# Kernel optimization log

Measured on AMD Instinct MI355X. Metric: run time of the kernel, lower is better.

## Reference

```python
import jax, jax.numpy as jnp
import numpy as np

EPS = 1e-5

def _layernorm(x, g, b):
    mu = jnp.mean(x, axis=-1, keepdims=True)
    var = jnp.mean(jnp.square(x - mu), axis=-1, keepdims=True)
    return (x - mu) * jax.lax.rsqrt(var + EPS) * g + b

def setup_inputs() -> dict:
    key = jax.random.key(0)
    B, N, C, MID = 1, 512, 128, 128
    ks = jax.random.split(key, 12)
    s_c = 1.0 / np.sqrt(C)
    s_m = 1.0 / np.sqrt(MID)
    return {
        "act": jax.random.normal(ks[0], (B, N, N, C), dtype=jnp.float32),
        "mask": jnp.ones((B, N, N), dtype=jnp.float32),
        # input LayerNorm
        "ln_in_g": jnp.ones((C,), jnp.float32),
        "ln_in_b": jnp.zeros((C,), jnp.float32),
        # left/right projections and gates (Linear: y = x @ W + b)
        "wl": jax.random.normal(ks[1], (C, MID), jnp.float32) * s_c,
        "bl": jnp.zeros((MID,), jnp.float32),
        "wr": jax.random.normal(ks[2], (C, MID), jnp.float32) * s_c,
        "br": jnp.zeros((MID,), jnp.float32),
        "wgl": jax.random.normal(ks[3], (C, MID), jnp.float32) * s_c,
        "bgl": jnp.zeros((MID,), jnp.float32),
        "wgr": jax.random.normal(ks[4], (C, MID), jnp.float32) * s_c,
        "bgr": jnp.zeros((MID,), jnp.float32),
        # output gating linear (C -> C)
        "wgate": jax.random.normal(ks[5], (C, C), jnp.float32) * s_c,
        "bgate": jnp.zeros((C,), jnp.float32),
        # center LayerNorm (over MID)
        "ln_c_g": jnp.ones((MID,), jnp.float32),
        "ln_c_b": jnp.zeros((MID,), jnp.float32),
        # output projection (MID -> C)
        "wout": jax.random.normal(ks[6], (MID, C), jnp.float32) * s_m,
        "bout": jnp.zeros((C,), jnp.float32),
    }

def reference(act, mask, ln_in_g, ln_in_b, wl, bl, wr, br, wgl, bgl, wgr, bgr,
              wgate, bgate, ln_c_g, ln_c_b, wout, bout):
    x = _layernorm(act, ln_in_g, ln_in_b)          # [B,N,N,C]
    m = mask[..., None]                             # [B,N,N,1]
    left_proj = m * (x @ wl + bl) * jax.nn.sigmoid(x @ wgl + bgl)   # [B,N,N,MID]
    right_proj = m * (x @ wr + br) * jax.nn.sigmoid(x @ wgr + bgr)  # [B,N,N,MID]
    gate_values = x @ wgate + bgate                 # [B,N,N,C]
    # triangle outgoing: contract over k (second index of both)
    out = jnp.einsum('bikc,bjkc->bijc', left_proj, right_proj)      # [B,N,N,MID]
    out = _layernorm(out, ln_c_g, ln_c_b)
    out = out @ wout + bout                         # [B,N,N,C]
    return out * jax.nn.sigmoid(gate_values)
```

## Files before the change

kernel.cpp:

```cpp
#include <hip/hip_runtime.h>

#define NPOS 512
#define NN_ (512 * 512)

typedef unsigned short u16;
typedef __attribute__((ext_vector_type(8))) short bf16x8_t;
typedef __attribute__((ext_vector_type(4))) float f32x4_t;

__device__ __forceinline__ float bf2f(u16 u) {
  union { unsigned int i; float f; } v;
  v.i = ((unsigned int)u) << 16;
  return v.f;
}
__device__ __forceinline__ u16 f2bf(float f) {
  __bf16 h = (__bf16)f;
  return __builtin_bit_cast(unsigned short, h);
}
__device__ __forceinline__ float sigm(float x) { return 1.0f / (1.0f + __expf(-x)); }

__device__ __forceinline__ void gld_lds16(u16* lds, const u16* g) {
  __builtin_amdgcn_global_load_lds(
      (const __attribute__((address_space(1))) unsigned int*)g,
      (__attribute__((address_space(3))) unsigned int*)lds, 16, 0, 0);
}

__global__ __launch_bounds__(256) void k0_wt(const float* __restrict__ wl,
                                             const float* __restrict__ wgl,
                                             const float* __restrict__ wr,
                                             const float* __restrict__ wgr,
                                             const float* __restrict__ wgate,
                                             u16* __restrict__ wtbase) {
  int b = blockIdx.x;
  int wi = b >> 3;
  int o0 = (b & 7) * 16;
  const float* W = wi == 0 ? wl : wi == 1 ? wgl : wi == 2 ? wr : wi == 3 ? wgr : wgate;
  u16* dst = wtbase + wi * 16384;
  int t = threadIdx.x;
  int o = o0 + (t >> 4);
  int k0 = (t & 15) * 8;
  float v[8];
#pragma unroll
  for (int i = 0; i < 8; ++i) v[i] = W[(k0 + i) * 128 + o];
  ushort4 a, b4;
  a.x = f2bf(v[0]); a.y = f2bf(v[1]); a.z = f2bf(v[2]); a.w = f2bf(v[3]);
  b4.x = f2bf(v[4]); b4.y = f2bf(v[5]); b4.z = f2bf(v[6]); b4.w = f2bf(v[7]);
  *(ushort4*)(dst + o * 128 + k0) = a;
  *(ushort4*)(dst + o * 128 + k0 + 4) = b4;
}

__global__ __launch_bounds__(256) void k0b(const float* __restrict__ wout,
                                           u16* __restrict__ Wt6) {
  int o = blockIdx.x * 16 + (threadIdx.x >> 4);
  int k0 = (threadIdx.x & 15) * 8;
  float v[8];
#pragma unroll
  for (int i = 0; i < 8; ++i) v[i] = wout[(k0 + i) * 128 + o];
  ushort4 a, b4;
  a.x = f2bf(v[0]); a.y = f2bf(v[1]); a.z = f2bf(v[2]); a.w = f2bf(v[3]);
  b4.x = f2bf(v[4]); b4.y = f2bf(v[5]); b4.z = f2bf(v[6]); b4.w = f2bf(v[7]);
  *(ushort4*)(Wt6 + o * 128 + k0) = a;
  *(ushort4*)(Wt6 + o * 128 + k0 + 4) = b4;
}

__global__ __launch_bounds__(512, 4) void k2_fused(
    const float* __restrict__ act, const float* __restrict__ mask,
    const u16* __restrict__ wtbase,
    const float* __restrict__ ln_g, const float* __restrict__ ln_b,
    const float* __restrict__ bl, const float* __restrict__ bgl,
    const float* __restrict__ br, const float* __restrict__ bgr,
    const float* __restrict__ bgate,
    u16* __restrict__ Lt, u16* __restrict__ Rt, u16* __restrict__ Gs) {
  __shared__ __align__(16) unsigned char smem[65536];
  u16* xn  = (u16*)smem;
  u16* wh0 = (u16*)(smem + 32768);
  u16* wh1 = (u16*)(smem + 49152);

  int tid = threadIdx.x;
  int l = tid & 63, w = tid >> 6;
  int wr_ = w >> 1, wc = w & 1;
  int lr = l & 15, lk = l >> 4;
  size_t p0 = (size_t)blockIdx.x * 128;

#define STAGE(i_, buf_)                                                     \
  {                                                                         \
    const u16* src = wtbase + ((i_) >> 1) * 16384 + ((i_) & 1) * 8192;      \
    _Pragma("unroll") for (int q = 0; q < 2; ++q) {                         \
      int s = q * 512 + tid;                                                \
      int row = s >> 4, j = (s & 15) ^ (row & 7);                           \
      gld_lds16((buf_) + s * 8, src + row * 128 + j * 8);                   \
    }                                                                       \
  }
#define ZERO(ACC)                                                           \
  { ACC[0][0] = (f32x4_t){0.f, 0.f, 0.f, 0.f};                              \
    ACC[0][1] = (f32x4_t){0.f, 0.f, 0.f, 0.f};                              \
    ACC[1][0] = (f32x4_t){0.f, 0.f, 0.f, 0.f};                              \
    ACC[1][1] = (f32x4_t){0.f, 0.f, 0.f, 0.f}; }
#define MFK(buf_, ACC, KT, AF0, AF1)                                        \
  {                                                                         \
    int kb = (KT) * 4 + lk;                                                 \
    int o0_ = wc * 32 + lr, o1_ = wc * 32 + 16 + lr;                        \
    bf16x8_t bfr0 = *(const bf16x8_t*)((buf_) + o0_ * 128 + ((kb ^ (o0_ & 7)) * 8)); \
    bf16x8_t bfr1 = *(const bf16x8_t*)((buf_) + o1_ * 128 + ((kb ^ (o1_ & 7)) * 8)); \
    ACC[0][0] = __builtin_amdgcn_mfma_f32_16x16x32_bf16(AF0, bfr0, ACC[0][0], 0, 0, 0); \
    ACC[0][1] = __builtin_amdgcn_mfma_f32_16x16x32_bf16(AF0, bfr1, ACC[0][1], 0, 0, 0); \
    ACC[1][0] = __builtin_amdgcn_mfma_f32_16x16x32_bf16(AF1, bfr0, ACC[1][0], 0, 0, 0); \
    ACC[1][1] = __builtin_amdgcn_mfma_f32_16x16x32_bf16(AF1, bfr1, ACC[1][1], 0, 0, 0); \
  }
#define MF(buf_, ACC)                                                       \
  MFK(buf_, ACC, 0, af00, af10)                                             \
  MFK(buf_, ACC, 1, af01, af11)                                             \
  MFK(buf_, ACC, 2, af02, af12)                                             \
  MFK(buf_, ACC, 3, af03, af13)
#define EPW(ACCP, ACCG, Bp_, Bg_, obase_, ob_)                              \
  {                                                                         \
    float bpv[2], bgv[2];                                                   \
    _Pragma("unroll") for (int n = 0; n < 2; ++n) {                         \
      int og = (obase_) + wc * 32 + n * 16 + lr;                            \
      bpv[n] = Bp_[og]; bgv[n] = Bg_[og];                                   \
    }                                                                       \
    _Pragma("unroll") for (int m = 0; m < 2; ++m) {                         \
      int p4 = wr_ * 32 + m * 16 + lk * 4;                                  \
      float4 mk = *(const float4*)(mask + p0 + p4);                         \
      int slot = p4 >> 3, off = p4 & 7;                                     \
      _Pragma("unroll") for (int n = 0; n < 2; ++n) {                       \
        int ol = wc * 32 + n * 16 + lr;                                     \
        ushort4 v;                                                          \
        v.x = f2bf(mk.x * (ACCP[m][n][0] + bpv[n]) * sigm(ACCG[m][n][0] + bgv[n])); \
        v.y = f2bf(mk.y * (ACCP[m][n][1] + bpv[n]) * sigm(ACCG[m][n][1] + bgv[n])); \
        v.z = f2bf(mk.z * (ACCP[m][n][2] + bpv[n]) * sigm(ACCG[m][n][2] + bgv[n])); \
        v.w = f2bf(mk.w * (ACCP[m][n][3] + bpv[n]) * sigm(ACCG[m][n][3] + bgv[n])); \
        *(ushort4*)((ob_) + ol * 128 + ((slot ^ (ol & 7)) << 3) + off) = v; \
      }                                                                     \
    }                                                                       \
  }
#define EPS(Tdst_, obase_, ob_)                                             \
  {                                                                         \
    _Pragma("unroll") for (int it = 0; it < 2; ++it) {                      \
      int s = it * 512 + tid;                                               \
      int ol = s >> 4, c8 = s & 15;                                         \
      *(uint4*)(Tdst_ + (size_t)((obase_) + ol) * NN_ + p0 + c8 * 8) =      \
          *(const uint4*)((ob_) + ol * 128 + ((c8 ^ (ol & 7)) << 3));       \
    }                                                                       \
  }

  STAGE(0, wh0);
  STAGE(1, wh1);

#pragma unroll
  for (int r = 0; r < 8; ++r) {
    int f = r * 512 + tid;
    int pos = f >> 5, c4 = f & 31;
    float4 v = *(const float4*)(act + (p0 + pos) * 128 + c4 * 4);
    float s1 = v.x + v.y + v.z + v.w;
    float s2 = v.x * v.x + v.y * v.y + v.z * v.z + v.w * v.w;
#pragma unroll
    for (int m = 1; m < 32; m <<= 1) {
      s1 += __shfl_xor(s1, m);
      s2 += __shfl_xor(s2, m);
    }
    float mu = s1 * (1.0f / 128.0f);
    float rstd = rsqrtf(s2 * (1.0f / 128.0f) - mu * mu + 1e-5f);
    int cb = c4 * 4;
    float4 gg = *(const float4*)(ln_g + cb);
    float4 bb = *(const float4*)(ln_b + cb);
    ushort4 o4;
    o4.x = f2bf((v.x - mu) * rstd * gg.x + bb.x);
    o4.y = f2bf((v.y - mu) * rstd * gg.y + bb.y);
    o4.z = f2bf((v.z - mu) * rstd * gg.z + bb.z);
    o4.w = f2bf((v.w - mu) * rstd * gg.w + bb.w);
    int c8 = c4 >> 1, off = (c4 & 1) * 4;
    *(ushort4*)(xn + pos * 128 + ((c8 ^ (pos & 7)) << 3) + off) = o4;
  }
  __syncthreads();

  bf16x8_t af00, af01, af02, af03, af10, af11, af12, af13;
  {
    int row0 = wr_ * 32 + lr;
    int row1 = wr_ * 32 + 16 + lr;
    const u16* x0 = xn + row0 * 128;
    const u16* x1 = xn + row1 * 128;
    af00 = *(const bf16x8_t*)(x0 + (((0 * 4 + lk) ^ (row0 & 7)) * 8));
    af01 = *(const bf16x8_t*)(x0 + (((1 * 4 + lk) ^ (row0 & 7)) * 8));
    af02 = *(const bf16x8_t*)(x0 + (((2 * 4 + lk) ^ (row0 & 7)) * 8));
    af03 = *(const bf16x8_t*)(x0 + (((3 * 4 + lk) ^ (row0 & 7)) * 8));
    af10 = *(const bf16x8_t*)(x1 + (((0 * 4 + lk) ^ (row1 & 7)) * 8));
    af11 = *(const bf16x8_t*)(x1 + (((1 * 4 + lk) ^ (row1 & 7)) * 8));
    af12 = *(const bf16x8_t*)(x1 + (((2 * 4 + lk) ^ (row1 & 7)) * 8));
    af13 = *(const bf16x8_t*)(x1 + (((3 * 4 + lk) ^ (row1 & 7)) * 8));
  }

  f32x4_t apA[2][2], apB[2][2], agA[2][2], agB[2][2];

  ZERO(apA); MF(wh0, apA);
  __syncthreads();
  STAGE(2, wh0);
  ZERO(apB); MF(wh1, apB);
  __syncthreads();
  STAGE(3, wh1);
  ZERO(agA); MF(wh0, agA);
  __syncthreads();
  STAGE(4, wh0);
  ZERO(agB); MF(wh1, agB);
  __syncthreads();
  EPW(apA, agA, bl, bgl, 0, wh1);
  __syncthreads();
  EPS(Lt, 0, wh1);
  __syncthreads();
  EPW(apB, agB, bl, bgl, 64, wh1);
  __syncthreads();
  EPS(Lt, 64, wh1);
  __syncthreads();

  STAGE(5, wh1);
  ZERO(apA); MF(wh0, apA);
  __syncthreads();
  STAGE(6, wh0);
  ZERO(apB); MF(wh1, apB);
  __syncthreads();
  STAGE(7, wh1);
  ZERO(agA); MF(wh0, agA);
  __syncthreads();
  STAGE(8, wh0);
  ZERO(agB); MF(wh1, agB);
  __syncthreads();
  EPW(apA, agA, br, bgr, 0, wh1);
  __syncthreads();
  EPS(Rt, 0, wh1);
  __syncthreads();
  EPW(apB, agB, br, bgr, 64, wh1);
  __syncthreads();
  EPS(Rt, 64, wh1);
  __syncthreads();

  STAGE(9, wh1);
  ZERO(apA); MF(wh0, apA);
  __syncthreads();
  ZERO(apB); MF(wh1, apB);
  __syncthreads();
  {
    u16* ob128 = wh0;
#pragma unroll
    for (int m = 0; m < 2; ++m) {
      int p4 = wr_ * 32 + m * 16 + lk * 4;
      int slot = p4 >> 3, off = p4 & 7;
#pragma unroll
      for (int n = 0; n < 2; ++n) {
        int oA = wc * 32 + n * 16 + lr;
        int oB = 64 + oA;
        float bA = bgate[oA], bB = bgate[oB];
        ushort4 vA, vB;
        vA.x = f2bf(apA[m][n][0] + bA); vA.y = f2bf(apA[m][n][1] + bA);
        vA.z = f2bf(apA[m][n][2] + bA); vA.w = f2bf(apA[m][n][3] + bA);
        vB.x = f2bf(apB[m][n][0] + bB); vB.y = f2bf(apB[m][n][1] + bB);
        vB.z = f2bf(apB[m][n][2] + bB); vB.w = f2bf(apB[m][n][3] + bB);
        *(ushort4*)(ob128 + oA * 128 + ((slot ^ (oA & 7)) << 3) + off) = vA;
        *(ushort4*)(ob128 + oB * 128 + ((slot ^ (oB & 7)) << 3) + off) = vB;
      }
    }
    __syncthreads();
#pragma unroll
    for (int it = 0; it < 4; ++it) {
      int s = it * 512 + tid;
      int o = s >> 4, c8 = s & 15;
      *(uint4*)(Gs + (size_t)o * NN_ + p0 + c8 * 8) =
          *(const uint4*)(ob128 + o * 128 + ((c8 ^ (o & 7)) << 3));
    }
  }
#undef STAGE
#undef ZERO
#undef MFK
#undef MF
#undef EPW
#undef EPS
}

__global__ __launch_bounds__(256, 4) void k3_einsum_mfma(const u16* __restrict__ Lt,
                                                         const u16* __restrict__ Rt,
                                                         u16* __restrict__ Ot) {
  __shared__ __align__(16) u16 smem[2 * 128 * 64];
  u16* La = smem;
  u16* Rb = smem + 128 * 64;

  int tid = threadIdx.x;
  int bid = blockIdx.x;
  int swz = (bid & 7) * 256 + (bid >> 3);
  int c = swz >> 4;
  int t = swz & 15;
  int i0 = (t >> 2) << 7, j0 = (t & 3) << 7;
  const u16* Lg = Lt + (size_t)c * NN_ + (size_t)i0 * 512;
  const u16* Rg = Rt + (size_t)c * NN_ + (size_t)j0 * 512;

  int l = tid & 63, w = tid >> 6;
  int wr = w >> 1, wc = w & 1;
  int lr = l & 15, lk = l >> 4;

  f32x4_t acc[4][4];
#pragma unroll
  for (int m = 0; m < 4; ++m)
#pragma unroll
    for (int n = 0; n < 4; ++n) acc[m][n] = (f32x4_t){0.f, 0.f, 0.f, 0.f};

  for (int kt = 0; kt < 512; kt += 64) {
#pragma unroll
    for (int q = 0; q < 4; ++q) {
      int s = q * 256 + tid;
      int row = s >> 3;
      int k8 = (s & 7) ^ (row & 7);
      gld_lds16(La + s * 8, Lg + (size_t)row * 512 + kt + k8 * 8);
      gld_lds16(Rb + s * 8, Rg + (size_t)row * 512 + kt + k8 * 8);
    }
    __syncthreads();

#pragma unroll
    for (int ks = 0; ks < 2; ++ks) {
      int kb = ks * 4 + lk;
      bf16x8_t af[4], bf[4];
#pragma unroll
      for (int m = 0; m < 4; ++m) {
        int row = wr * 64 + m * 16 + lr;
        af[m] = *(const bf16x8_t*)(La + row * 64 + ((kb ^ (row & 7)) * 8));
      }
#pragma unroll
      for (int n = 0; n < 4; ++n) {
        int row = wc * 64 + n * 16 + lr;
        bf[n] = *(const bf16x8_t*)(Rb + row * 64 + ((kb ^ (row & 7)) * 8));
      }
#pragma unroll
      for (int m = 0; m < 4; ++m)
#pragma unroll
        for (int n = 0; n < 4; ++n)
          acc[m][n] = __builtin_amdgcn_mfma_f32_16x16x32_bf16(af[m], bf[n], acc[m][n], 0, 0, 0);
    }
    __syncthreads();
  }

  u16* ob = smem;
#pragma unroll
  for (int m = 0; m < 4; ++m) {
    int row0 = wr * 64 + m * 16 + lk * 4;
#pragma unroll
    for (int n = 0; n < 4; ++n) {
      int col = (wc * 64 + n * 16 + lr) ^ (lk << 4);
#pragma unroll
      for (int r = 0; r < 4; ++r)
        ob[(row0 + r) * 128 + col] = f2bf(acc[m][n][r]);
    }
  }
  __syncthreads();
#pragma unroll
  for (int it = 0; it < 8; ++it) {
    int s = it * 256 + tid;
    int row = s >> 4, c8 = s & 15;
    int g = (row >> 2) & 3;
    const u16* src = ob + row * 128 + ((c8 * 8) ^ (g << 4));
    *(uint4*)(Ot + (size_t)c * NN_ + (size_t)(i0 + row) * 512 + j0 + c8 * 8) =
        *(const uint4*)src;
  }
}

__global__ __launch_bounds__(512, 4) void k4_mfma(const u16* __restrict__ Ot,
                                                  const u16* __restrict__ Gs,
                                                  const u16* __restrict__ Wt6,
                                                  const float* __restrict__ gc,
                                                  const float* __restrict__ bc,
                                                  const float* __restrict__ bout,
                                                  float* __restrict__ out) {
  __shared__ __align__(16) unsigned char smem[70656];
  u16* ot = (u16*)smem;
  u16* ws = (u16*)(smem + 32768);
  float* ps = (float*)(smem + 65536);
  float* pss = (float*)(smem + 67584);
  float2* munr = (float2*)(smem + 69632);

  int tid = threadIdx.x;
  int l = tid & 63, w = tid >> 6;
  int wr = w >> 1, wc = w & 1;
  int lr = l & 15, lk = l >> 4;
  size_t p0 = (size_t)blockIdx.x * 128;
  int i_row = (int)(p0 >> 9);
  int j0 = (int)(p0 & 511);

#pragma unroll
  for (int q = 0; q < 4; ++q) {
    int s = q * 512 + tid;
    int cc = s >> 4, j = s & 15;
    gld_lds16(ot + s * 8, Ot + (size_t)cc * NN_ + (size_t)i_row * 512 + j0 + j * 8);
  }
#pragma unroll
  for (int q = 0; q < 4; ++q) {
    int s = q * 512 + tid;
    int o = s >> 4, j = (s & 15) ^ (o & 7);
    gld_lds16(ws + s * 8, Wt6 + o * 128 + j * 8);
  }
  __syncthreads();

  int g = tid >> 7, pos = tid & 127;
  float vals[32];
  float s1 = 0.0f, s2 = 0.0f;
#pragma unroll
  for (int m = 0; m < 32; ++m) {
    float v = bf2f(ot[(g * 32 + m) * 128 + pos]);
    vals[m] = v;
    s1 += v;
    s2 += v * v;
  }
  ps[g * 128 + pos] = s1;
  pss[g * 128 + pos] = s2;
  __syncthreads();
  if (tid < 128) {
    float a = ps[tid] + ps[128 + tid] + ps[256 + tid] + ps[384 + tid];
    float b = pss[tid] + pss[128 + tid] + pss[256 + tid] + pss[384 + tid];
    float mu = a * (1.0f / 128.0f);
    float rstd = rsqrtf(b * (1.0f / 128.0f) - mu * mu + 1e-5f);
    munr[tid] = make_float2(mu, rstd);
  }
  __syncthreads();
  float2 mr = munr[pos];

  u16* xn = ot;
#pragma unroll
  for (int mm = 0; mm < 4; ++mm) {
    int c8 = g * 4 + mm;
    ushort4 va, vb;
    int cb = c8 * 8;
    va.x = f2bf((vals[mm * 8 + 0] - mr.x) * mr.y * gc[cb + 0] + bc[cb + 0]);
    va.y = f2bf((vals[mm * 8 + 1] - mr.x) * mr.y * gc[cb + 1] + bc[cb + 1]);
    va.z = f2bf((vals[mm * 8 + 2] - mr.x) * mr.y * gc[cb + 2] + bc[cb + 2]);
    va.w = f2bf((vals[mm * 8 + 3] - mr.x) * mr.y * gc[cb + 3] + bc[cb + 3]);
    vb.x = f2bf((vals[mm * 8 + 4] - mr.x) * mr.y * gc[cb + 4] + bc[cb + 4]);
    vb.y = f2bf((vals[mm * 8 + 5] - mr.x) * mr.y * gc[cb + 5] + bc[cb + 5]);
    vb.z = f2bf((vals[mm * 8 + 6] - mr.x) * mr.y * gc[cb + 6] + bc[cb + 6]);
    vb.w = f2bf((vals[mm * 8 + 7] - mr.x) * mr.y * gc[cb + 7] + bc[cb + 7]);
    int slot = (c8 ^ (pos & 7)) * 8;
    *(ushort4*)(xn + pos * 128 + slot) = va;
    *(ushort4*)(xn + pos * 128 + slot + 4) = vb;
  }
  __syncthreads();

  f32x4_t acc[2][4];
#pragma unroll
  for (int m = 0; m < 2; ++m)
#pragma unroll
    for (int n = 0; n < 4; ++n) acc[m][n] = (f32x4_t){0.f, 0.f, 0.f, 0.f};

#pragma unroll
  for (int kt = 0; kt < 4; ++kt) {
    int kb = kt * 4 + lk;
    bf16x8_t af[2], bf[4];
#pragma unroll
    for (int m = 0; m < 2; ++m) {
      int row = wr * 32 + m * 16 + lr;
      af[m] = *(const bf16x8_t*)(xn + row * 128 + ((kb ^ (row & 7)) * 8));
    }
#pragma unroll
    for (int n = 0; n < 4; ++n) {
      int o = wc * 64 + n * 16 + lr;
      bf[n] = *(const bf16x8_t*)(ws + o * 128 + ((kb ^ (o & 7)) * 8));
    }
#pragma unroll
    for (int m = 0; m < 2; ++m)
#pragma unroll
      for (int n = 0; n < 4; ++n)
        acc[m][n] = __builtin_amdgcn_mfma_f32_16x16x32_bf16(af[m], bf[n], acc[m][n], 0, 0, 0);
  }

  float* os = (float*)(smem + 32768);
#pragma unroll
  for (int h = 0; h < 2; ++h) {
    __syncthreads();
    if ((wr >> 1) == h) {
      int rb = (wr & 1) * 32;
#pragma unroll
      for (int n = 0; n < 4; ++n) {
        int o = wc * 64 + n * 16 + lr;
        float bo = bout[o];
#pragma unroll
        for (int m = 0; m < 2; ++m) {
          int p = rb + m * 16 + lk * 4;
          ushort4 g4 = *(const ushort4*)(Gs + (size_t)o * NN_ + p0 + h * 64 + p);
          float gv[4] = {sigm(bf2f(g4.x)), sigm(bf2f(g4.y)),
                         sigm(bf2f(g4.z)), sigm(bf2f(g4.w))};
#pragma unroll
          for (int r = 0; r < 4; ++r) {
            int row = p + r;
            os[row * 128 + (o ^ (((row >> 2) & 7) << 4))] = (acc[m][n][r] + bo) * gv[r];
          }
        }
      }
    }
    __syncthreads();
#pragma unroll
    for (int it = 0; it < 4; ++it) {
      int s = it * 512 + tid;
      int row = s >> 5, sl = s & 31;
      float4 v = *(const float4*)(os + row * 128 + ((sl * 4) ^ (((row >> 2) & 7) << 4)));
      *(float4*)(out + (p0 + h * 64 + row) * 128 + sl * 4) = v;
    }
  }
}

extern "C" void kernel_launch(void* const* d_in, const int* in_sizes, int n_in,
                              void* d_out, int out_size, void* d_ws, size_t ws_size,
                              hipStream_t stream) {
  const float* act    = (const float*)d_in[0];
  const float* mask   = (const float*)d_in[1];
  const float* ln_in_g = (const float*)d_in[2];
  const float* ln_in_b = (const float*)d_in[3];
  const float* wl     = (const float*)d_in[4];
  const float* bl     = (const float*)d_in[5];
  const float* wr     = (const float*)d_in[6];
  const float* br     = (const float*)d_in[7];
  const float* wgl    = (const float*)d_in[8];
  const float* bgl    = (const float*)d_in[9];
  const float* wgr    = (const float*)d_in[10];
  const float* bgr    = (const float*)d_in[11];
  const float* wgate  = (const float*)d_in[12];
  const float* bgate  = (const float*)d_in[13];
  const float* ln_c_g = (const float*)d_in[14];
  const float* ln_c_b = (const float*)d_in[15];
  const float* wout   = (const float*)d_in[16];
  const float* bout   = (const float*)d_in[17];
  float* out = (float*)d_out;

  char* ws = (char*)d_ws;
  const size_t SEG = 1ull << 26;
  u16* Lt  = (u16*)(ws);
  u16* Rt  = (u16*)(ws + 1 * SEG);
  u16* Gs  = (u16*)(ws + 2 * SEG);
  u16* Ot  = (u16*)(ws + 3 * SEG);
  u16* Wt6 = Lt;

  u16* wtbase = (u16*)((char*)d_out + (size_t)out_size * 4 - 5 * 32768);

  k0_wt<<<dim3(40), dim3(256), 0, stream>>>(wl, wgl, wr, wgr, wgate, wtbase);
  k2_fused<<<dim3(2048), dim3(512), 0, stream>>>(act, mask, wtbase, ln_in_g, ln_in_b,
                                                 bl, bgl, br, bgr, bgate, Lt, Rt, Gs);
  k3_einsum_mfma<<<dim3(2048), dim3(256), 0, stream>>>(Lt, Rt, Ot);
  k0b<<<dim3(8), dim3(256), 0, stream>>>(wout, Wt6);
  k4_mfma<<<dim3(2048), dim3(512), 0, stream>>>(Ot, Gs, Wt6, ln_c_g, ln_c_b, bout, out);
}
```

Before: 299.7 us.

## Reorder projection staging and add dedicated LDS output buffer in fused k2

The fused projection kernel now computes each projection and its gate half back-to-back, so only two accumulator sets stay live instead of four. The weight-staging order is changed to match. A separate 16KB LDS output buffer is added, so epilogue writes and global stores no longer reuse weight buffers. This lets the next weight stages be issued before the epilogue and removes several __syncthreads. The cost is LDS per block growing from 64KB to 80KB, which may limit how many blocks fit on a CU.

```diff
diff --git a/kernel.cpp b/kernel.cpp
--- a/kernel.cpp
+++ b/kernel.cpp
@@ -70,10 +70,11 @@
     const float* __restrict__ br, const float* __restrict__ bgr,
     const float* __restrict__ bgate,
     u16* __restrict__ Lt, u16* __restrict__ Rt, u16* __restrict__ Gs) {
-  __shared__ __align__(16) unsigned char smem[65536];
+  __shared__ __align__(16) unsigned char smem[81920];
   u16* xn  = (u16*)smem;
   u16* wh0 = (u16*)(smem + 32768);
   u16* wh1 = (u16*)(smem + 49152);
+  u16* ob  = (u16*)(smem + 65536);
 
   int tid = threadIdx.x;
   int l = tid & 63, w = tid >> 6;
@@ -111,7 +112,7 @@
   MFK(buf_, ACC, 1, af01, af11)                                             \
   MFK(buf_, ACC, 2, af02, af12)                                             \
   MFK(buf_, ACC, 3, af03, af13)
-#define EPW(ACCP, ACCG, Bp_, Bg_, obase_, ob_)                              \
+#define EPW(ACCP, ACCG, Bp_, Bg_, obase_)                                   \
   {                                                                         \
     float bpv[2], bgv[2];                                                   \
     _Pragma("unroll") for (int n = 0; n < 2; ++n) {                         \
@@ -129,22 +130,41 @@
         v.y = f2bf(mk.y * (ACCP[m][n][1] + bpv[n]) * sigm(ACCG[m][n][1] + bgv[n])); \
         v.z = f2bf(mk.z * (ACCP[m][n][2] + bpv[n]) * sigm(ACCG[m][n][2] + bgv[n])); \
         v.w = f2bf(mk.w * (ACCP[m][n][3] + bpv[n]) * sigm(ACCG[m][n][3] + bgv[n])); \
-        *(ushort4*)((ob_) + ol * 128 + ((slot ^ (ol & 7)) << 3) + off) = v; \
+        *(ushort4*)(ob + ol * 128 + ((slot ^ (ol & 7)) << 3) + off) = v;    \
       }                                                                     \
     }                                                                       \
   }
-#define EPS(Tdst_, obase_, ob_)                                             \
+#define GEPW(ACC, obase_)                                                   \
+  {                                                                         \
+    float bgv[2];                                                           \
+    _Pragma("unroll") for (int n = 0; n < 2; ++n)                           \
+      bgv[n] = bgate[(obase_) + wc * 32 + n * 16 + lr];                     \
+    _Pragma("unroll") for (int m = 0; m < 2; ++m) {                         \
+      int p4 = wr_ * 32 + m * 16 + lk * 4;                                  \
+      int slot = p4 >> 3, off = p4 & 7;                                     \
+      _Pragma("unroll") for (int n = 0; n < 2; ++n) {                       \
+        int ol = wc * 32 + n * 16 + lr;                                     \
+        ushort4 v;                                                          \
+        v.x = f2bf(ACC[m][n][0] + bgv[n]);                                  \
+        v.y = f2bf(ACC[m][n][1] + bgv[n]);                                  \
+        v.z = f2bf(ACC[m][n][2] + bgv[n]);                                  \
+        v.w = f2bf(ACC[m][n][3] + bgv[n]);                                  \
+        *(ushort4*)(ob + ol * 128 + ((slot ^ (ol & 7)) << 3) + off) = v;    \
+      }                                                                     \
+    }                                                                       \
+  }
+#define EPS(Tdst_, obase_)                                                  \
   {                                                                         \
     _Pragma("unroll") for (int it = 0; it < 2; ++it) {                      \
       int s = it * 512 + tid;                                               \
       int ol = s >> 4, c8 = s & 15;                                         \
       *(uint4*)(Tdst_ + (size_t)((obase_) + ol) * NN_ + p0 + c8 * 8) =      \
-          *(const uint4*)((ob_) + ol * 128 + ((c8 ^ (ol & 7)) << 3));       \
+          *(const uint4*)(ob + ol * 128 + ((c8 ^ (ol & 7)) << 3));          \
     }                                                                       \
   }
 
   STAGE(0, wh0);
-  STAGE(1, wh1);
+  STAGE(2, wh1);
 
 #pragma unroll
   for (int r = 0; r < 8; ++r) {
@@ -189,88 +209,60 @@
     af13 = *(const bf16x8_t*)(x1 + (((3 * 4 + lk) ^ (row1 & 7)) * 8));
   }
 
-  f32x4_t apA[2][2], apB[2][2], agA[2][2], agB[2][2];
-
-  ZERO(apA); MF(wh0, apA);
-  __syncthreads();
-  STAGE(2, wh0);
-  ZERO(apB); MF(wh1, apB);
-  __syncthreads();
+  f32x4_t ap[2][2], ag[2][2];
+
+  ZERO(ap); MF(wh0, ap);
+  ZERO(ag); MF(wh1, ag);
+  __syncthreads();
+  STAGE(1, wh0);
   STAGE(3, wh1);
-  ZERO(agA); MF(wh0, agA);
+  EPW(ap, ag, bl, bgl, 0);
+  __syncthreads();
+  EPS(Lt, 0);
+
+  ZERO(ap); MF(wh0, ap);
+  ZERO(ag); MF(wh1, ag);
   __syncthreads();
   STAGE(4, wh0);
-  ZERO(agB); MF(wh1, agB);
-  __syncthreads();
-  EPW(apA, agA, bl, bgl, 0, wh1);
-  __syncthreads();
-  EPS(Lt, 0, wh1);
-  __syncthreads();
-  EPW(apB, agB, bl, bgl, 64, wh1);
-  __syncthreads();
-  EPS(Lt, 64, wh1);
-  __syncthreads();
-
-  STAGE(5, wh1);
-  ZERO(apA); MF(wh0, apA);
-  __syncthreads();
-  STAGE(6, wh0);
-  ZERO(apB); MF(wh1, apB);
-  __syncthreads();
+  STAGE(6, wh1);
+  EPW(ap, ag, bl, bgl, 64);
+  __syncthreads();
+  EPS(Lt, 64);
+
+  ZERO(ap); MF(wh0, ap);
+  ZERO(ag); MF(wh1, ag);
+  __syncthreads();
+  STAGE(5, wh0);
   STAGE(7, wh1);
-  ZERO(agA); MF(wh0, agA);
+  EPW(ap, ag, br, bgr, 0);
+  __syncthreads();
+  EPS(Rt, 0);
+
+  ZERO(ap); MF(wh0, ap);
+  ZERO(ag); MF(wh1, ag);
   __syncthreads();
   STAGE(8, wh0);
-  ZERO(agB); MF(wh1, agB);
-  __syncthreads();
-  EPW(apA, agA, br, bgr, 0, wh1);
-  __syncthreads();
-  EPS(Rt, 0, wh1);
-  __syncthreads();
-  EPW(apB, agB, br, bgr, 64, wh1);
-  __syncthreads();
-  EPS(Rt, 64, wh1);
-  __syncthreads();
-
   STAGE(9, wh1);
-  ZERO(apA); MF(wh0, apA);
-  __syncthreads();
-  ZERO(apB); MF(wh1, apB);
-  __syncthreads();
-  {
-    u16* ob128 = wh0;
-#pragma unroll
-    for (int m = 0; m < 2; ++m) {
-      int p4 = wr_ * 32 + m * 16 + lk * 4;
-      int slot = p4 >> 3, off = p4 & 7;
-#pragma unroll
-      for (int n = 0; n < 2; ++n) {
-        int oA = wc * 32 + n * 16 + lr;
-        int oB = 64 + oA;
-        float bA = bgate[oA], bB = bgate[oB];
-        ushort4 vA, vB;
-        vA.x = f2bf(apA[m][n][0] + bA); vA.y = f2bf(apA[m][n][1] + bA);
-        vA.z = f2bf(apA[m][n][2] + bA); vA.w = f2bf(apA[m][n][3] + bA);
-        vB.x = f2bf(apB[m][n][0] + bB); vB.y = f2bf(apB[m][n][1] + bB);
-        vB.z = f2bf(apB[m][n][2] + bB); vB.w = f2bf(apB[m][n][3] + bB);
-        *(ushort4*)(ob128 + oA * 128 + ((slot ^ (oA & 7)) << 3) + off) = vA;
-        *(ushort4*)(ob128 + oB * 128 + ((slot ^ (oB & 7)) << 3) + off) = vB;
-      }
-    }
-    __syncthreads();
-#pragma unroll
-    for (int it = 0; it < 4; ++it) {
-      int s = it * 512 + tid;
-      int o = s >> 4, c8 = s & 15;
-      *(uint4*)(Gs + (size_t)o * NN_ + p0 + c8 * 8) =
-          *(const uint4*)(ob128 + o * 128 + ((c8 ^ (o & 7)) << 3));
-    }
-  }
+  EPW(ap, ag, br, bgr, 64);
+  __syncthreads();
+  EPS(Rt, 64);
+
+  ZERO(ap); MF(wh0, ap);
+  ZERO(ag); MF(wh1, ag);
+  __syncthreads();
+  GEPW(ap, 0);
+  __syncthreads();
+  EPS(Gs, 0);
+  __syncthreads();
+  GEPW(ag, 64);
+  __syncthreads();
+  EPS(Gs, 64);
 #undef STAGE
 #undef ZERO
 #undef MFK
 #undef MF
 #undef EPW
+#undef GEPW
 #undef EPS
 }
 
```

After: 266.1 us. 11.2% less time.
